# Kernel tuning notes

Measured on AMD Instinct MI355X. Metric: run time of the kernel, lower is better.

The kernel has to match this reference:

```python
import jax, jax.numpy as jnp
import numpy as np

NUM_BASIS = 9  # ADVANCED_LIB in oikan: x, x^2, x^3, exp, log(|x|+1), sqrt(|x|), tanh, sin, abs


def _basis(x):
    # x: [B, Din] -> [B, Din, K] basis expansion matching ADVANCED_LIB
    ax = jnp.abs(x)
    return jnp.stack([
        x,
        x * x,
        x * x * x,
        jnp.exp(x),
        jnp.log(ax + 1.0),
        jnp.sqrt(ax),
        jnp.tanh(x),
        jnp.sin(x),
        ax,
    ], axis=-1)


def setup_inputs() -> dict:
    key = jax.random.key(0)
    k1, k2, k3 = jax.random.split(key, 3)
    B, Din, Dout, K = 4096, 128, 128, NUM_BASIS
    x = jax.random.normal(k1, (B, Din), dtype=jnp.float32)
    # per-edge basis weights (SymbolicEdge.weights ~ randn)
    W = jax.random.normal(k2, (Din, Dout, K), dtype=jnp.float32)
    # per-edge bias (initialized to zeros in SymbolicEdge)
    bias = jnp.zeros((Din, Dout), dtype=jnp.float32)
    # combination_weights ~ 0.1 * randn
    C = jax.random.normal(k3, (Din, Dout), dtype=jnp.float32) * 0.1
    return {"x": x, "W": W, "bias": bias, "C": C}


def reference(x, W, bias, C):
    feats = _basis(x)  # [B, Din, K]
    # edge_outputs[b, i, o] = sum_k feats[b,i,k] * W[i,o,k] + bias[i,o]
    edge = jnp.einsum('bik,iok->bio', feats, W) + bias  # [B, Din, Dout]
    # combined sum over input dim with combination weights
    return jnp.einsum('bio,io->bo', edge, C)  # [B, Dout]
```

## Files before the change

kernel.cpp:

```cpp
#include <hip/hip_runtime.h>
#include <math.h>


#define DIN   128
#define DOUT  128
#define NB    9
#define KK    (DIN * NB)
#define BATCH 4096
#define ROWS  16
#define APAD  8
#define ASTR  (KK + APAD)

typedef __bf16 bf16x8 __attribute__((ext_vector_type(8)));
typedef float  f32x4  __attribute__((ext_vector_type(4)));
typedef unsigned int uint;

__device__ __forceinline__ uint pack2(float lo, float hi) {
    __bf16 l = (__bf16)lo, h = (__bf16)hi;
    unsigned short ul, uh;
    __builtin_memcpy(&ul, &l, 2);
    __builtin_memcpy(&uh, &h, 2);
    return (uint)ul | ((uint)uh << 16);
}

__device__ __forceinline__ void basis9(float v, float* f) {
    const float av = fabsf(v);
    f[0] = v;
    f[1] = v * v;
    f[2] = f[1] * v;
    f[3] = __expf(v);
    f[4] = __logf(av + 1.0f);
    f[5] = __builtin_sqrtf(av);
    const float e2 = __expf(-2.0f * av);
    const float th = (1.0f - e2) * __builtin_amdgcn_rcpf(1.0f + e2);
    f[6] = __builtin_copysignf(th, v);
    f[7] = __sinf(v);
    f[8] = av;
}

__global__ __launch_bounds__(256) void fold_kernel(const float* __restrict__ W,
                                                   const float* __restrict__ bias,
                                                   const float* __restrict__ C,
                                                   __bf16* __restrict__ BT,
                                                   float* __restrict__ bterm) {
    const int b = blockIdx.x;
    const int t = threadIdx.x;

    if (b < 32) {
        const int e2 = b * 256 + t;
        const int o  = e2 >> 6;
        const int ip = e2 & 63;
        const int i  = ip * 2;

        const float c0 = C[i * DOUT + o];
        const float c1 = C[(i + 1) * DOUT + o];
        const float* w0 = W + ((size_t)i * DOUT + o) * NB;
        const float* w1 = W + ((size_t)(i + 1) * DOUT + o) * NB;

        float f[18];
        #pragma unroll
        for (int k = 0; k < NB; ++k) f[k]      = w0[k] * c0;
        #pragma unroll
        for (int k = 0; k < NB; ++k) f[NB + k] = w1[k] * c1;

        uint* dst = (uint*)(BT + (size_t)o * KK + i * NB);
        #pragma unroll
        for (int j = 0; j < 9; ++j) dst[j] = pack2(f[2 * j], f[2 * j + 1]);
    } else {
        const int o = b - 32;
        float p = 0.0f;
        if (t < DIN) p = bias[t * DOUT + o] * C[t * DOUT + o];
        p += __shfl_down(p, 32);
        p += __shfl_down(p, 16);
        p += __shfl_down(p, 8);
        p += __shfl_down(p, 4);
        p += __shfl_down(p, 2);
        p += __shfl_down(p, 1);
        __shared__ float red[4];
        if ((t & 63) == 0) red[t >> 6] = p;
        __syncthreads();
        if (t == 0) bterm[o] = red[0] + red[1] + red[2] + red[3];
    }
}

__global__ __launch_bounds__(512, 1) void fused_kernel(const float* __restrict__ x,
                                                       const __bf16* __restrict__ BT,
                                                       const float* __restrict__ bterm,
                                                       float* __restrict__ out) {
    __shared__ __bf16 As[ROWS * ASTR];
    const int t    = threadIdx.x;
    const int row0 = blockIdx.x * ROWS;

    const int lane = t & 63;
    const int wave = t >> 6;
    const int m    = lane & 15;
    const int quad = lane >> 4;
    const int col0 = wave << 4;
    const float bt = bterm[col0 + m];

    #pragma unroll
    for (int pp = 0; pp < 2; ++pp) {
        const int p  = t + pp * 512;
        const int r  = p >> 6;
        const int ip = p & 63;
        const int i  = ip * 2;
        const float2 xv = *(const float2*)&x[(size_t)(row0 + r) * DIN + i];
        float fa[9], fb[9];
        basis9(xv.x, fa);
        basis9(xv.y, fb);
        uint* dst = (uint*)&As[r * ASTR + i * NB];
        dst[0] = pack2(fa[0], fa[1]);
        dst[1] = pack2(fa[2], fa[3]);
        dst[2] = pack2(fa[4], fa[5]);
        dst[3] = pack2(fa[6], fa[7]);
        dst[4] = pack2(fa[8], fb[0]);
        dst[5] = pack2(fb[1], fb[2]);
        dst[6] = pack2(fb[3], fb[4]);
        dst[7] = pack2(fb[5], fb[6]);
        dst[8] = pack2(fb[7], fb[8]);
    }
    __syncthreads();

    const __bf16* Ap = &As[m * ASTR + quad * 8];
    const __bf16* Bp = BT + (size_t)(col0 + m) * KK + quad * 8;

    f32x4 acc = {0.0f, 0.0f, 0.0f, 0.0f};

    #pragma unroll 6
    for (int kc = 0; kc < KK / 32; ++kc) {
        bf16x8 a = *(const bf16x8*)(Ap + kc * 32);
        bf16x8 b = *(const bf16x8*)(Bp + kc * 32);
        acc = __builtin_amdgcn_mfma_f32_16x16x32_bf16(a, b, acc, 0, 0, 0);
    }

    float* op = out + (size_t)(row0 + quad * 4) * DOUT + col0 + m;
    #pragma unroll
    for (int r = 0; r < 4; ++r) op[(size_t)r * DOUT] = acc[r] + bt;
}

extern "C" void kernel_launch(void* const* d_in, const int* in_sizes, int n_in,
                              void* d_out, int out_size, void* d_ws, size_t ws_size,
                              hipStream_t stream) {
    const float* x    = (const float*)d_in[0];
    const float* W    = (const float*)d_in[1];
    const float* bias = (const float*)d_in[2];
    const float* C    = (const float*)d_in[3];
    float* out = (float*)d_out;

    char* ws = (char*)d_ws;
    __bf16* BT    = (__bf16*)ws;
    float*  bterm = (float*)(ws + (size_t)DOUT * KK * 2);

    fold_kernel<<<160, 256, 0, stream>>>(W, bias, C, BT, bterm);
    fused_kernel<<<BATCH / ROWS, 512, 0, stream>>>(x, BT, bterm, out);
}
```

Before: 71.98 us.

## Fuse weight folding into a single tiled K-chunked KAN GEMM kernel

Drops the separate fold kernel and its workspace round-trip. A single kernel now works on 64-row by 32-column output tiles and loops over four input-dimension chunks. In each chunk it builds the bf16 basis tile for x and the C-scaled weight tile in shared memory, then runs MFMA on them. The bias term is reduced inside each block. This saves a kernel launch and the global write and read of the folded B matrix. The cost is that each block recomputes the basis features and reloads W with strided, poorly coalesced accesses, and there is a sync per chunk.

```diff
diff --git a/kernel.cpp b/kernel.cpp
--- a/kernel.cpp
+++ b/kernel.cpp
@@ -7,9 +7,13 @@
 #define NB    9
 #define KK    (DIN * NB)
 #define BATCH 4096
-#define ROWS  16
-#define APAD  8
-#define ASTR  (KK + APAD)
+#define BR    64
+#define BC    32
+#define IC    32
+#define BK    (IC * NB)
+#define NCH   (DIN / IC)
+#define PAD   8
+#define LSTR  (BK + PAD)
 
 typedef __bf16 bf16x8 __attribute__((ext_vector_type(8)));
 typedef float  f32x4  __attribute__((ext_vector_type(4)));
@@ -38,102 +42,106 @@
     f[8] = av;
 }
 
-__global__ __launch_bounds__(256) void fold_kernel(const float* __restrict__ W,
-                                                   const float* __restrict__ bias,
-                                                   const float* __restrict__ C,
-                                                   __bf16* __restrict__ BT,
-                                                   float* __restrict__ bterm) {
-    const int b = blockIdx.x;
-    const int t = threadIdx.x;
+__global__ __launch_bounds__(512, 1) void kan_kernel(const float* __restrict__ x,
+                                                     const float* __restrict__ W,
+                                                     const float* __restrict__ bias,
+                                                     const float* __restrict__ C,
+                                                     float* __restrict__ out) {
+    __shared__ __bf16 As[BR * LSTR];
+    __shared__ __bf16 Bs[BC * LSTR];
+    __shared__ float  btl[BC];
 
-    if (b < 32) {
-        const int e2 = b * 256 + t;
-        const int o  = e2 >> 6;
-        const int ip = e2 & 63;
-        const int i  = ip * 2;
+    const int t    = threadIdx.x;
+    const int rb   = blockIdx.x >> 2;
+    const int cb   = blockIdx.x & 3;
+    const int row0 = rb * BR;
+    const int col0 = cb * BC;
 
-        const float c0 = C[i * DOUT + o];
-        const float c1 = C[(i + 1) * DOUT + o];
-        const float* w0 = W + ((size_t)i * DOUT + o) * NB;
-        const float* w1 = W + ((size_t)(i + 1) * DOUT + o) * NB;
+    const int lane = t & 63;
+    const int wave = t >> 6;
+    const int wr   = wave & 3;
+    const int wc   = wave >> 2;
+    const int m    = lane & 15;
+    const int quad = lane >> 4;
 
-        float f[18];
+    {
+        const int o_l = t >> 4;
+        const int ig  = t & 15;
+        const int o   = col0 + o_l;
+        float p = 0.0f;
         #pragma unroll
-        for (int k = 0; k < NB; ++k) f[k]      = w0[k] * c0;
-        #pragma unroll
-        for (int k = 0; k < NB; ++k) f[NB + k] = w1[k] * c1;
-
-        uint* dst = (uint*)(BT + (size_t)o * KK + i * NB);
-        #pragma unroll
-        for (int j = 0; j < 9; ++j) dst[j] = pack2(f[2 * j], f[2 * j + 1]);
-    } else {
-        const int o = b - 32;
-        float p = 0.0f;
-        if (t < DIN) p = bias[t * DOUT + o] * C[t * DOUT + o];
-        p += __shfl_down(p, 32);
-        p += __shfl_down(p, 16);
+        for (int s = 0; s < 8; ++s) {
+            const int i = ig * 8 + s;
+            p += bias[i * DOUT + o] * C[i * DOUT + o];
+        }
         p += __shfl_down(p, 8);
         p += __shfl_down(p, 4);
         p += __shfl_down(p, 2);
         p += __shfl_down(p, 1);
-        __shared__ float red[4];
-        if ((t & 63) == 0) red[t >> 6] = p;
-        __syncthreads();
-        if (t == 0) bterm[o] = red[0] + red[1] + red[2] + red[3];
+        if (ig == 0) btl[o_l] = p;
     }
-}
-
-__global__ __launch_bounds__(512, 1) void fused_kernel(const float* __restrict__ x,
-                                                       const __bf16* __restrict__ BT,
-                                                       const float* __restrict__ bterm,
-                                                       float* __restrict__ out) {
-    __shared__ __bf16 As[ROWS * ASTR];
-    const int t    = threadIdx.x;
-    const int row0 = blockIdx.x * ROWS;
-
-    const int lane = t & 63;
-    const int wave = t >> 6;
-    const int m    = lane & 15;
-    const int quad = lane >> 4;
-    const int col0 = wave << 4;
-    const float bt = bterm[col0 + m];
-
-    #pragma unroll
-    for (int pp = 0; pp < 2; ++pp) {
-        const int p  = t + pp * 512;
-        const int r  = p >> 6;
-        const int ip = p & 63;
-        const int i  = ip * 2;
-        const float2 xv = *(const float2*)&x[(size_t)(row0 + r) * DIN + i];
-        float fa[9], fb[9];
-        basis9(xv.x, fa);
-        basis9(xv.y, fb);
-        uint* dst = (uint*)&As[r * ASTR + i * NB];
-        dst[0] = pack2(fa[0], fa[1]);
-        dst[1] = pack2(fa[2], fa[3]);
-        dst[2] = pack2(fa[4], fa[5]);
-        dst[3] = pack2(fa[6], fa[7]);
-        dst[4] = pack2(fa[8], fb[0]);
-        dst[5] = pack2(fb[1], fb[2]);
-        dst[6] = pack2(fb[3], fb[4]);
-        dst[7] = pack2(fb[5], fb[6]);
-        dst[8] = pack2(fb[7], fb[8]);
-    }
-    __syncthreads();
-
-    const __bf16* Ap = &As[m * ASTR + quad * 8];
-    const __bf16* Bp = BT + (size_t)(col0 + m) * KK + quad * 8;
 
     f32x4 acc = {0.0f, 0.0f, 0.0f, 0.0f};
+    const __bf16* Ap = &As[(wr * 16 + m) * LSTR + quad * 8];
+    const __bf16* Bp = &Bs[(wc * 16 + m) * LSTR + quad * 8];
 
-    #pragma unroll 6
-    for (int kc = 0; kc < KK / 32; ++kc) {
-        bf16x8 a = *(const bf16x8*)(Ap + kc * 32);
-        bf16x8 b = *(const bf16x8*)(Bp + kc * 32);
-        acc = __builtin_amdgcn_mfma_f32_16x16x32_bf16(a, b, acc, 0, 0, 0);
+    for (int ck = 0; ck < NCH; ++ck) {
+        const int ib0 = ck * IC;
+
+        #pragma unroll
+        for (int pp = 0; pp < 2; ++pp) {
+            const int p  = t + pp * 512;
+            const int r  = p >> 4;
+            const int il = (p & 15) * 2;
+            const float2 xv = *(const float2*)&x[(size_t)(row0 + r) * DIN + ib0 + il];
+            float fa[9], fb[9];
+            basis9(xv.x, fa);
+            basis9(xv.y, fb);
+            uint* dst = (uint*)&As[r * LSTR + il * NB];
+            dst[0] = pack2(fa[0], fa[1]);
+            dst[1] = pack2(fa[2], fa[3]);
+            dst[2] = pack2(fa[4], fa[5]);
+            dst[3] = pack2(fa[6], fa[7]);
+            dst[4] = pack2(fa[8], fb[0]);
+            dst[5] = pack2(fb[1], fb[2]);
+            dst[6] = pack2(fb[3], fb[4]);
+            dst[7] = pack2(fb[5], fb[6]);
+            dst[8] = pack2(fb[7], fb[8]);
+        }
+
+        {
+            const int o_l = t >> 4;
+            const int il  = (t & 15) * 2;
+            const int i   = ib0 + il;
+            const int o   = col0 + o_l;
+            const float c0 = C[i * DOUT + o];
+            const float c1 = C[(i + 1) * DOUT + o];
+            const float* w0 = W + ((size_t)i * DOUT + o) * NB;
+            const float* w1 = W + ((size_t)(i + 1) * DOUT + o) * NB;
+            float f[18];
+            #pragma unroll
+            for (int k = 0; k < NB; ++k) f[k]      = w0[k] * c0;
+            #pragma unroll
+            for (int k = 0; k < NB; ++k) f[NB + k] = w1[k] * c1;
+            uint* dst = (uint*)&Bs[o_l * LSTR + il * NB];
+            #pragma unroll
+            for (int j = 0; j < 9; ++j) dst[j] = pack2(f[2 * j], f[2 * j + 1]);
+        }
+
+        __syncthreads();
+
+        #pragma unroll
+        for (int j = 0; j < BK / 32; ++j) {
+            bf16x8 a = *(const bf16x8*)(Ap + j * 32);
+            bf16x8 b = *(const bf16x8*)(Bp + j * 32);
+            acc = __builtin_amdgcn_mfma_f32_16x16x32_bf16(a, b, acc, 0, 0, 0);
+        }
+
+        if (ck + 1 < NCH) __syncthreads();
     }
 
-    float* op = out + (size_t)(row0 + quad * 4) * DOUT + col0 + m;
+    const float bt = btl[wc * 16 + m];
+    float* op = out + (size_t)(row0 + wr * 16 + quad * 4) * DOUT + col0 + wc * 16 + m;
     #pragma unroll
     for (int r = 0; r < 4; ++r) op[(size_t)r * DOUT] = acc[r] + bt;
 }
@@ -147,10 +155,5 @@
     const float* C    = (const float*)d_in[3];
     float* out = (float*)d_out;
 
-    char* ws = (char*)d_ws;
-    __bf16* BT    = (__bf16*)ws;
-    float*  bterm = (float*)(ws + (size_t)DOUT * KK * 2);
-
-    fold_kernel<<<160, 256, 0, stream>>>(W, bias, C, BT, bterm);
-    fused_kernel<<<BATCH / ROWS, 512, 0, stream>>>(x, BT, bterm, out);
+    kan_kernel<<<(BATCH / BR) * (DOUT / BC), 512, 0, stream>>>(x, W, bias, C, out);
 }
```

Measured after the change: 76.42 us. 6.2% more time.
